# Kernel optimization log

Hardware: AMD Instinct MI355X
Metric: run time of the kernel (lower is better)

The kernel has to match this reference:

```python
import jax, jax.numpy as jnp
import numpy as np

B, N, D, K, E = 64, 512, 16, 16, 128
LN_EPS = 1e-5


def _layernorm(h, g, b):
    m = jnp.mean(h, axis=-1, keepdims=True)
    v = jnp.mean(jnp.square(h - m), axis=-1, keepdims=True)
    return (h - m) * jax.lax.rsqrt(v + LN_EPS) * g + b


def _linear_init(key, fan_in, fan_out):
    s = 1.0 / np.sqrt(fan_in)
    kw, kb = jax.random.split(key)
    W = jax.random.uniform(kw, (fan_in, fan_out), jnp.float32, -s, s)
    b = jax.random.uniform(kb, (fan_out,), jnp.float32, -s, s)
    return W, b


def setup_inputs() -> dict:
    key = jax.random.key(0)
    ks = jax.random.split(key, 4)
    x = jax.random.normal(ks[0], (B, N, D), jnp.float32)
    W1, b1 = _linear_init(ks[1], 2 * D, E)
    W2, b2 = _linear_init(ks[2], E, E)
    W3, b3 = _linear_init(ks[3], E, E)
    ones, zeros = jnp.ones((E,), jnp.float32), jnp.zeros((E,), jnp.float32)
    return {
        "x": x,
        "W1": W1, "b1": b1, "g1": ones, "be1": zeros,
        "W2": W2, "b2": b2, "g2": ones, "be2": zeros,
        "W3": W3, "b3": b3, "g3": ones, "be3": zeros,
    }


def reference(x, W1, b1, g1, be1, W2, b2, g2, be2, W3, b3, g3, be3):
    # kNN on coordinate features (columns 8, 9)
    xy = x[..., 8:10]                                   # [B, N, 2]
    d2 = jnp.sum(jnp.square(xy[:, :, None, :] - xy[:, None, :, :]), axis=-1)  # [B, N, N]
    _, idx = jax.lax.top_k(-d2, K)                      # smallest distances -> [B, N, K]

    # gather neighbor features per batch
    neighbors = jax.vmap(lambda xb, ib: xb[ib])(x, idx)  # [B, N, K, D]
    central = jnp.broadcast_to(x[:, :, None, :], (B, N, K, D))
    feats = jnp.concatenate([central, neighbors - central], axis=-1)  # [B, N, K, 2D]

    h = jax.nn.gelu(_layernorm(feats @ W1 + b1, g1, be1), approximate=False)
    h = jax.nn.gelu(_layernorm(h @ W2 + b2, g2, be2), approximate=False)
    h = jax.nn.gelu(_layernorm(h @ W3 + b3, g3, be3), approximate=False)  # [B, N, K, E]

    return jnp.mean(h, axis=2)                          # [B, N, E]
```

## Files before the change

kernel.cpp:

```cpp
#include <hip/hip_runtime.h>
#include <math.h>

#define Bdim 64
#define Ndim 512
#define Ddim 16
#define Kdim 16
#define Edim 128
#define LN_EPS 1e-5f

#define PTS   2
#define NT    8
#define KS2   4

typedef __attribute__((ext_vector_type(8))) short bf16x8;
typedef __attribute__((ext_vector_type(4))) float f32x4;

__device__ __forceinline__ unsigned short f2bf(float f) {
    unsigned u = __float_as_uint(f);
    unsigned r = (u + 0x7FFFu + ((u >> 16) & 1u)) >> 16;
    return (unsigned short)r;
}

__device__ __forceinline__ float gelu_fast(float x) {
    float x2 = x * x;
    float t  = fmaf(x2, -0.0713548162f, -1.5957691216f);
    float e  = __expf(x * t);
    return x * __builtin_amdgcn_rcpf(1.0f + e);
}

__global__ __launch_bounds__(256) void pack_w_kernel(
    const float* __restrict__ W1, const float* __restrict__ W2,
    const float* __restrict__ W3, unsigned short* __restrict__ wp)
{
    int idx = blockIdx.x * 256 + threadIdx.x;
    if (idx >= 36864) return;
    if (idx < 4096) {
        int t = idx;
        int nt = t >> 9, l = (t >> 3) & 63, j = t & 7;
        int k = 8 * (l >> 4) + j, n = nt * 16 + (l & 15);
        wp[idx] = f2bf(W1[k * Edim + n]);
    } else if (idx < 20480) {
        int t = idx - 4096;
        int nt = t >> 11, ks = (t >> 9) & 3, l = (t >> 3) & 63, j = t & 7;
        int k = ks * 32 + 8 * (l >> 4) + j, n = nt * 16 + (l & 15);
        wp[idx] = f2bf(W2[k * Edim + n]);
    } else {
        int t = idx - 20480;
        int nt = t >> 11, ks = (t >> 9) & 3, l = (t >> 3) & 63, j = t & 7;
        int k = ks * 32 + 8 * (l >> 4) + j, n = nt * 16 + (l & 15);
        wp[idx] = f2bf(W3[k * Edim + n]);
    }
}

__device__ __forceinline__ void ln_gelu_acc(
    f32x4 acc[NT], const float* __restrict__ g, const float* __restrict__ be, int lane)
{
    const int cl = lane & 15;
    float s[4] = {0.f,0.f,0.f,0.f}, s2[4] = {0.f,0.f,0.f,0.f};
    #pragma unroll
    for (int nt = 0; nt < NT; ++nt)
        #pragma unroll
        for (int j = 0; j < 4; ++j) {
            float v = acc[nt][j];
            s[j] += v;
            s2[j] = fmaf(v, v, s2[j]);
        }
    #pragma unroll
    for (int off = 1; off < 16; off <<= 1)
        #pragma unroll
        for (int j = 0; j < 4; ++j) {
            s[j]  += __shfl_xor(s[j],  off, 64);
            s2[j] += __shfl_xor(s2[j], off, 64);
        }
    float mj[4], rj[4];
    #pragma unroll
    for (int j = 0; j < 4; ++j) {
        float m   = s[j]  * (1.0f/128.0f);
        float var = s2[j] * (1.0f/128.0f) - m * m;
        mj[j] = m;
        rj[j] = __builtin_amdgcn_rsqf(var + LN_EPS);
    }
    #pragma unroll
    for (int nt = 0; nt < NT; ++nt) {
        const float gv = g[nt*16 + cl], bev = be[nt*16 + cl];
        #pragma unroll
        for (int j = 0; j < 4; ++j) {
            float v = (acc[nt][j] - mj[j]) * rj[j];
            v = fmaf(v, gv, bev);
            acc[nt][j] = gelu_fast(v);
        }
    }
}

__device__ __forceinline__ void store_h(
    const f32x4 acc[NT], unsigned short* __restrict__ s_h, int wave, int lane)
{
    const int cl = lane & 15, gq = lane >> 4;
    const int rbase = 16*wave + 4*gq;
    #pragma unroll
    for (int nt = 0; nt < NT; ++nt) {
        const int col = nt*16 + cl;
        const int cb  = col >> 3;
        #pragma unroll
        for (int j = 0; j < 4; ++j) {
            const int row = rbase + j;
            s_h[row*128 + ((cb ^ (row & 7)) << 3) + (col & 7)] = f2bf(acc[nt][j]);
        }
    }
}

__global__ __launch_bounds__(128, 4) void edgeconv_mfma(
    const float* __restrict__ x,
    const unsigned short* __restrict__ wp,
    const float* __restrict__ b1, const float* __restrict__ g1, const float* __restrict__ be1,
    const float* __restrict__ b2, const float* __restrict__ g2, const float* __restrict__ be2,
    const float* __restrict__ b3, const float* __restrict__ g3, const float* __restrict__ be3,
    float* __restrict__ out)
{
    const int tid  = threadIdx.x;
    const int wave = tid >> 6, lane = tid & 63;
    const int bp = blockIdx.x;
    const int b  = bp >> 8;
    const int n0 = (bp & 255) * PTS;
    const int n  = n0 + wave;

    __shared__ __align__(16) unsigned short s_h[32 * 128];

    const float* __restrict__ xb = x + (size_t)b * (Ndim * Ddim);
    const int cl = lane & 15, gq = lane >> 4;

    float cxr[8], cyr[8];
    #pragma unroll
    for (int c = 0; c < 8; ++c) {
        const float2 p2 = *(const float2*)(xb + (c * 64 + lane) * Ddim + 8);
        cxr[c] = p2.x; cyr[c] = p2.y;
    }

    unsigned my_nb = 0;
    {
        const float qx = xb[n * Ddim + 8], qy = xb[n * Ddim + 9];
        unsigned long long key[8];
        #pragma unroll
        for (int c = 0; c < 8; ++c) {
            int j = c * 64 + lane;
            float dx = __fsub_rn(qx, cxr[c]);
            float dy = __fsub_rn(qy, cyr[c]);
            float d2 = __fadd_rn(__fmul_rn(dx,dx), __fmul_rn(dy,dy));
            key[c] = ((unsigned long long)__float_as_uint(d2) << 32) | (unsigned)j;
        }
        for (int sel = 0; sel < Kdim; ++sel) {
            unsigned long long m = key[0];
            #pragma unroll
            for (int c = 1; c < 8; ++c) m = (key[c] < m) ? key[c] : m;
            #pragma unroll
            for (int off = 32; off > 0; off >>= 1) {
                unsigned long long o = __shfl_xor(m, off, 64);
                m = (o < m) ? o : m;
            }
            unsigned widx = (unsigned)m;
            if ((lane & 15) == sel) my_nb = widx;
            const bool owner = ((widx & 63u) == (unsigned)lane);
            const unsigned co = widx >> 6;
            #pragma unroll
            for (int c = 0; c < 8; ++c)
                if (owner && co == (unsigned)c) key[c] = ~0ull;
        }
    }

    f32x4 acc[NT];

    {
        const int off8 = (gq & 1) * 8;
        const float* pc = xb + n * Ddim + off8;
        const float* pn = xb + (int)my_nb * Ddim + off8;
        float4 c0 = *(const float4*)(pc);
        float4 c1 = *(const float4*)(pc + 4);
        float4 v0 = *(const float4*)(pn);
        float4 v1 = *(const float4*)(pn + 4);
        const bool diff = (gq >= 2);
        float e0 = diff ? (v0.x - c0.x) : c0.x;
        float e1 = diff ? (v0.y - c0.y) : c0.y;
        float e2 = diff ? (v0.z - c0.z) : c0.z;
        float e3 = diff ? (v0.w - c0.w) : c0.w;
        float e4 = diff ? (v1.x - c1.x) : c1.x;
        float e5 = diff ? (v1.y - c1.y) : c1.y;
        float e6 = diff ? (v1.z - c1.z) : c1.z;
        float e7 = diff ? (v1.w - c1.w) : c1.w;
        bf16x8 a1;
        a1[0] = (short)f2bf(e0); a1[1] = (short)f2bf(e1);
        a1[2] = (short)f2bf(e2); a1[3] = (short)f2bf(e3);
        a1[4] = (short)f2bf(e4); a1[5] = (short)f2bf(e5);
        a1[6] = (short)f2bf(e6); a1[7] = (short)f2bf(e7);

        #pragma unroll
        for (int nt = 0; nt < NT; ++nt) {
            const float bv = b1[nt*16 + cl];
            bf16x8 bfr = *(const bf16x8*)(wp + (nt*64 + lane)*8);
            f32x4 c = {bv, bv, bv, bv};
            acc[nt] = __builtin_amdgcn_mfma_f32_16x16x32_bf16(a1, bfr, c, 0, 0, 0);
        }
    }
    ln_gelu_acc(acc, g1, be1, lane);
    store_h(acc, s_h, wave, lane);

    #pragma unroll 1
    for (int layer = 0; layer < 2; ++layer) {
        const unsigned short* wpL = wp + (layer == 0 ? 4096 : 20480);
        const float* bL  = (layer == 0) ? b2  : b3;
        const float* gL  = (layer == 0) ? g2  : g3;
        const float* beL = (layer == 0) ? be2 : be3;

        bf16x8 a[KS2];
        {
            const int row = 16*wave + cl;
            #pragma unroll
            for (int ks = 0; ks < KS2; ++ks) {
                const int cb = ks*4 + gq;
                a[ks] = *(const bf16x8*)(&s_h[row*128 + ((cb ^ (row & 7)) << 3)]);
            }
        }
        #pragma unroll
        for (int nt = 0; nt < NT; ++nt) {
            const float bv = bL[nt*16 + cl];
            f32x4 c = {bv, bv, bv, bv};
            #pragma unroll
            for (int ks = 0; ks < KS2; ++ks) {
                bf16x8 bfr = *(const bf16x8*)(wpL + ((nt*KS2 + ks)*64 + lane)*8);
                c = __builtin_amdgcn_mfma_f32_16x16x32_bf16(a[ks], bfr, c, 0, 0, 0);
            }
            acc[nt] = c;
        }
        ln_gelu_acc(acc, gL, beL, lane);
        if (layer == 0) store_h(acc, s_h, wave, lane);
    }

    #pragma unroll
    for (int nt = 0; nt < NT; ++nt) {
        float sv = acc[nt][0] + acc[nt][1] + acc[nt][2] + acc[nt][3];
        sv += __shfl_xor(sv, 16, 64);
        sv += __shfl_xor(sv, 32, 64);
        if (gq == (nt >> 1))
            out[((size_t)b * Ndim + n) * Edim + nt*16 + cl] = sv * (1.0f/16.0f);
    }
}

extern "C" void kernel_launch(void* const* d_in, const int* in_sizes, int n_in,
                              void* d_out, int out_size, void* d_ws, size_t ws_size,
                              hipStream_t stream)
{
    const float* x   = (const float*)d_in[0];
    const float* W1  = (const float*)d_in[1];
    const float* b1  = (const float*)d_in[2];
    const float* g1  = (const float*)d_in[3];
    const float* be1 = (const float*)d_in[4];
    const float* W2  = (const float*)d_in[5];
    const float* b2  = (const float*)d_in[6];
    const float* g2  = (const float*)d_in[7];
    const float* be2 = (const float*)d_in[8];
    const float* W3  = (const float*)d_in[9];
    const float* b3  = (const float*)d_in[10];
    const float* g3  = (const float*)d_in[11];
    const float* be3 = (const float*)d_in[12];
    float* out = (float*)d_out;
    unsigned short* wp = (unsigned short*)d_ws;

    hipLaunchKernelGGL(pack_w_kernel, dim3(144), dim3(256), 0, stream, W1, W2, W3, wp);
    hipLaunchKernelGGL(edgeconv_mfma, dim3((Bdim * Ndim) / PTS), dim3(128), 0, stream,
                       x, wp, b1, g1, be1, b2, g2, be2, b3, g3, be3, out);
}
```

Before: 196.2 us.

## Sort per-lane kNN keys, use hardware bf16 pack and exp2 in GELU

Each lane's eight distance keys are sorted once with a sorting network, so every top-k round reads key[0] directly and the owning lane shifts its list instead of doing a linear min and a masked clear. Coordinate loads now happen inside the distance loop rather than being preloaded into registers. Bf16 conversion now uses the v_cvt_pk_bf16_f32 instruction in place of the software rounding routine. GELU folds the log2(e) factor into its constants and calls exp2 directly. This cuts ALU work in the selection and activation paths, but depends on the packed-convert instruction being available and on its rounding matching the software version.

```diff
diff --git a/kernel.cpp b/kernel.cpp
--- a/kernel.cpp
+++ b/kernel.cpp
@@ -15,16 +15,28 @@
 typedef __attribute__((ext_vector_type(8))) short bf16x8;
 typedef __attribute__((ext_vector_type(4))) float f32x4;
 
+#if __has_builtin(__builtin_amdgcn_exp2f)
+#define EXP2F __builtin_amdgcn_exp2f
+#else
+#define EXP2F exp2f
+#endif
+
 __device__ __forceinline__ unsigned short f2bf(float f) {
     unsigned u = __float_as_uint(f);
     unsigned r = (u + 0x7FFFu + ((u >> 16) & 1u)) >> 16;
     return (unsigned short)r;
 }
 
+__device__ __forceinline__ unsigned cvt_pk_bf16(float a, float b) {
+    unsigned r;
+    asm("v_cvt_pk_bf16_f32 %0, %1, %2" : "=v"(r) : "v"(a), "v"(b));
+    return r;
+}
+
 __device__ __forceinline__ float gelu_fast(float x) {
     float x2 = x * x;
-    float t  = fmaf(x2, -0.0713548162f, -1.5957691216f);
-    float e  = __expf(x * t);
+    float t  = fmaf(x2, -0.10294324f, -2.30220821f);
+    float e  = EXP2F(x * t);
     return x * __builtin_amdgcn_rcpf(1.0f + e);
 }
 
@@ -101,11 +113,16 @@
     for (int nt = 0; nt < NT; ++nt) {
         const int col = nt*16 + cl;
         const int cb  = col >> 3;
-        #pragma unroll
-        for (int j = 0; j < 4; ++j) {
-            const int row = rbase + j;
-            s_h[row*128 + ((cb ^ (row & 7)) << 3) + (col & 7)] = f2bf(acc[nt][j]);
-        }
+        const unsigned r01 = cvt_pk_bf16(acc[nt][0], acc[nt][1]);
+        const unsigned r23 = cvt_pk_bf16(acc[nt][2], acc[nt][3]);
+        const int a0 = (rbase+0)*128 + ((cb ^ ((rbase+0) & 7)) << 3) + (col & 7);
+        const int a1 = (rbase+1)*128 + ((cb ^ ((rbase+1) & 7)) << 3) + (col & 7);
+        const int a2 = (rbase+2)*128 + ((cb ^ ((rbase+2) & 7)) << 3) + (col & 7);
+        const int a3 = (rbase+3)*128 + ((cb ^ ((rbase+3) & 7)) << 3) + (col & 7);
+        s_h[a0] = (unsigned short)(r01 & 0xFFFFu);
+        s_h[a1] = (unsigned short)(r01 >> 16);
+        s_h[a2] = (unsigned short)(r23 & 0xFFFFu);
+        s_h[a3] = (unsigned short)(r23 >> 16);
     }
 }
 
@@ -129,13 +146,6 @@
     const float* __restrict__ xb = x + (size_t)b * (Ndim * Ddim);
     const int cl = lane & 15, gq = lane >> 4;
 
-    float cxr[8], cyr[8];
-    #pragma unroll
-    for (int c = 0; c < 8; ++c) {
-        const float2 p2 = *(const float2*)(xb + (c * 64 + lane) * Ddim + 8);
-        cxr[c] = p2.x; cyr[c] = p2.y;
-    }
-
     unsigned my_nb = 0;
     {
         const float qx = xb[n * Ddim + 8], qy = xb[n * Ddim + 9];
@@ -143,15 +153,26 @@
         #pragma unroll
         for (int c = 0; c < 8; ++c) {
             int j = c * 64 + lane;
-            float dx = __fsub_rn(qx, cxr[c]);
-            float dy = __fsub_rn(qy, cyr[c]);
+            const float2 p2 = *(const float2*)(xb + j * Ddim + 8);
+            float dx = __fsub_rn(qx, p2.x);
+            float dy = __fsub_rn(qy, p2.y);
             float d2 = __fadd_rn(__fmul_rn(dx,dx), __fmul_rn(dy,dy));
             key[c] = ((unsigned long long)__float_as_uint(d2) << 32) | (unsigned)j;
         }
+        #define CE(A,B) { bool c_ = key[A] < key[B];                          \
+                          unsigned long long lo_ = c_ ? key[A] : key[B];      \
+                          unsigned long long hi_ = c_ ? key[B] : key[A];      \
+                          key[A] = lo_; key[B] = hi_; }
+        CE(0,1) CE(2,3) CE(4,5) CE(6,7)
+        CE(0,2) CE(1,3) CE(4,6) CE(5,7)
+        CE(1,2) CE(5,6)
+        CE(0,4) CE(1,5) CE(2,6) CE(3,7)
+        CE(2,4) CE(3,5)
+        CE(1,2) CE(3,4) CE(5,6)
+        #undef CE
+
         for (int sel = 0; sel < Kdim; ++sel) {
             unsigned long long m = key[0];
-            #pragma unroll
-            for (int c = 1; c < 8; ++c) m = (key[c] < m) ? key[c] : m;
             #pragma unroll
             for (int off = 32; off > 0; off >>= 1) {
                 unsigned long long o = __shfl_xor(m, off, 64);
@@ -160,10 +181,10 @@
             unsigned widx = (unsigned)m;
             if ((lane & 15) == sel) my_nb = widx;
             const bool owner = ((widx & 63u) == (unsigned)lane);
-            const unsigned co = widx >> 6;
-            #pragma unroll
-            for (int c = 0; c < 8; ++c)
-                if (owner && co == (unsigned)c) key[c] = ~0ull;
+            if (owner) {
+                key[0] = key[1]; key[1] = key[2]; key[2] = key[3]; key[3] = key[4];
+                key[4] = key[5]; key[5] = key[6]; key[6] = key[7]; key[7] = ~0ull;
+            }
         }
     }
 
@@ -186,11 +207,12 @@
         float e5 = diff ? (v1.y - c1.y) : c1.y;
         float e6 = diff ? (v1.z - c1.z) : c1.z;
         float e7 = diff ? (v1.w - c1.w) : c1.w;
-        bf16x8 a1;
-        a1[0] = (short)f2bf(e0); a1[1] = (short)f2bf(e1);
-        a1[2] = (short)f2bf(e2); a1[3] = (short)f2bf(e3);
-        a1[4] = (short)f2bf(e4); a1[5] = (short)f2bf(e5);
-        a1[6] = (short)f2bf(e6); a1[7] = (short)f2bf(e7);
+        union { unsigned u[4]; bf16x8 v; } a1u;
+        a1u.u[0] = cvt_pk_bf16(e0, e1);
+        a1u.u[1] = cvt_pk_bf16(e2, e3);
+        a1u.u[2] = cvt_pk_bf16(e4, e5);
+        a1u.u[3] = cvt_pk_bf16(e6, e7);
+        const bf16x8 a1 = a1u.v;
 
         #pragma unroll
         for (int nt = 0; nt < NT; ++nt) {
```

Result: slower. 211.1 us (+7.6%).
